# Kernel tuning notes

Measured on AMD Instinct MI355X. Metric: run time of the kernel, lower is better.

Reference implementation:

```python
import jax, jax.numpy as jnp
import numpy as np

N = 100_000        # total nodes (BN)
E = 1_600_000      # directed edges before bidirectionalization
B = 8              # graphs in batch
CFG = 1000         # configs per graph -> BC = 8000
N_OPS = 120
OP_EMB = 8
F_NODE = 140
H = 64
IN_DIMS = [F_NODE + OP_EMB, H, H]  # [148, 64, 64]


def setup_inputs() -> dict:
    key = jax.random.key(0)
    ks = iter(jax.random.split(key, 40))
    d = {}
    d["node_feat"] = jax.random.normal(next(ks), (N, F_NODE), dtype=jnp.float32)
    d["node_opcode"] = jax.random.randint(next(ks), (N,), 0, N_OPS)
    d["edge_index"] = jax.random.randint(next(ks), (E, 2), 0, N)
    d["config_feat"] = jax.random.normal(next(ks), (B * CFG, 24), dtype=jnp.float32)
    d["n_configs"] = jnp.full((B,), CFG, dtype=jnp.int32)
    d["batch"] = jnp.repeat(jnp.arange(B, dtype=jnp.int32), N // B)
    d["op_emb"] = jax.random.normal(next(ks), (N_OPS, OP_EMB), dtype=jnp.float32) * 0.1
    s = 0.05
    for l, din in enumerate(IN_DIMS):
        d[f"sage_wl{l}"] = jax.random.normal(next(ks), (din, din), dtype=jnp.float32) * s
        d[f"sage_bl{l}"] = jnp.zeros((din,), dtype=jnp.float32)
        d[f"sage_wr{l}"] = jax.random.normal(next(ks), (din, din), dtype=jnp.float32) * s
        d[f"lin_w{l}"] = jax.random.normal(next(ks), (2 * din, H), dtype=jnp.float32) * s
        d[f"lin_b{l}"] = jnp.zeros((H,), dtype=jnp.float32)
    d["post_w1"] = jax.random.normal(next(ks), (H + 24, H), dtype=jnp.float32) * s
    d["post_b1"] = jnp.zeros((H,), dtype=jnp.float32)
    d["post_w2"] = jax.random.normal(next(ks), (H, 1), dtype=jnp.float32) * s
    d["post_b2"] = jnp.zeros((1,), dtype=jnp.float32)
    return d


def _forward(node_feat, config_feat, op_emb, layer_params, post_w1, post_b1,
             post_w2, post_b2, node_opcode, edge_index, n_configs, batch):
    # Bidirectional edges: original + transposed (matches edge_index[..., [1,0]] cat)
    src = jnp.concatenate([edge_index[:, 0], edge_index[:, 1]])
    dst = jnp.concatenate([edge_index[:, 1], edge_index[:, 0]])
    deg = jax.ops.segment_sum(jnp.ones_like(dst, dtype=node_feat.dtype), dst,
                              num_segments=N)
    inv_deg = (1.0 / jnp.maximum(deg, 1.0))[:, None]  # zero-in-degree -> mean 0

    x = jnp.concatenate([node_feat, op_emb[node_opcode]], axis=-1)  # (N, 148)
    for (wl, bl, wr, lw, lb) in layer_params:
        # SAGEConv: mean-aggregate neighbor messages, + root transform
        agg = jax.ops.segment_sum(x[src], dst, num_segments=N) * inv_deg
        h = agg @ wl + bl + x @ wr
        # normalize=True -> L2 normalize (F.normalize, eps=1e-12)
        nrm = jnp.linalg.norm(h, axis=-1, keepdims=True)
        h = h / jnp.maximum(nrm, 1e-12)
        z = jnp.concatenate([h, x], axis=-1) @ lw + lb
        x = jax.nn.leaky_relu(z)  # negative_slope=0.01 as in torch default

    g = jax.ops.segment_sum(x, batch, num_segments=B)  # global_add_pool (B, 64)
    g = jnp.repeat(g, n_configs, axis=0, total_repeat_length=B * CFG)
    z = jnp.concatenate([g, config_feat], axis=-1)     # (BC, 88)
    z = jax.nn.leaky_relu(z @ post_w1 + post_b1)
    out = (z @ post_w2 + post_b2).squeeze(-1)          # (BC,)
    return out


def reference(node_feat, node_opcode, edge_index, config_feat, n_configs, batch,
              op_emb,
              sage_wl0, sage_bl0, sage_wr0, lin_w0, lin_b0,
              sage_wl1, sage_bl1, sage_wr1, lin_w1, lin_b1,
              sage_wl2, sage_bl2, sage_wr2, lin_w2, lin_b2,
              post_w1, post_b1, post_w2, post_b2):
    layer_params = [
        (sage_wl0, sage_bl0, sage_wr0, lin_w0, lin_b0),
        (sage_wl1, sage_bl1, sage_wr1, lin_w1, lin_b1),
        (sage_wl2, sage_bl2, sage_wr2, lin_w2, lin_b2),
    ]
    return _forward(node_feat, config_feat, op_emb, layer_params,
                    post_w1, post_b1, post_w2, post_b2,
                    node_opcode, edge_index, n_configs, batch)
```

## Files before the change

kernel.cpp:

```cpp
#include <hip/hip_runtime.h>
#include <cstdint>
#include <cstddef>


#define LRELU(v) ((v) > 0.f ? (v) : 0.01f * (v))

typedef __attribute__((ext_vector_type(8))) short bf16x8;
typedef __attribute__((ext_vector_type(4))) float f32x4;
typedef float floatx2 __attribute__((ext_vector_type(2)));

union U4B8 {
    uint4 u;
    bf16x8 b;
};

__device__ inline unsigned bf16_rn(float x) {
    unsigned u = __float_as_uint(x);
    return (u + 0x7fffu + ((u >> 16) & 1u)) >> 16;
}
__device__ inline unsigned pack2(float lo, float hi) {
    return bf16_rn(lo) | (bf16_rn(hi) << 16);
}
__device__ inline float2 up2(unsigned v) {
    return make_float2(__uint_as_float(v << 16), __uint_as_float(v & 0xffff0000u));
}

__device__ inline float e4m3_to_f32(unsigned b) {
    float v = __uint_as_float((b & 0x7fu) << 20) * 0x1p120f;
    return __uint_as_float(__float_as_uint(v) | ((b & 0x80u) << 24));
}

template <bool HI>
__device__ inline floatx2 fp8x2_dec(unsigned v) {
#if __has_builtin(__builtin_amdgcn_cvt_pk_f32_fp8)
    return __builtin_amdgcn_cvt_pk_f32_fp8((int)v, HI);
#else
    unsigned w = HI ? (v >> 16) : v;
    floatx2 r;
    r.x = e4m3_to_f32(w & 0xffu);
    r.y = e4m3_to_f32((w >> 8) & 0xffu);
    return r;
#endif
}

__device__ inline unsigned char f32_to_e4m3_sw(float f) {
    unsigned u = __float_as_uint(f);
    unsigned s = (u >> 24) & 0x80u;
    float a = fabsf(f);
    if (a > 448.f) a = 448.f;
    unsigned b = __float_as_uint(a);
    int exp = (int)(b >> 23) - 127;
    unsigned r;
    if (exp < -9) {
        r = 0;
    } else if (exp >= -6) {
        unsigned m = b & 0x7fffffu;
        unsigned keep = m >> 20;
        unsigned rb = (m >> 19) & 1u;
        unsigned sticky = (m & 0x7ffffu) ? 1u : 0u;
        unsigned inc = rb & (sticky | (keep & 1u));
        unsigned em = (((unsigned)(exp + 7)) << 3) | keep;
        em += inc;
        if (em > 0x7eu) em = 0x7eu;
        r = em;
    } else {
        float t = a * 512.f;
        int q = (int)(t + 0.5f);
        r = (q > 7) ? 0x08u : (unsigned)q;
    }
    return (unsigned char)(r | s);
}

__device__ inline unsigned fp8x4_enc(float f0, float f1, float f2, float f3) {
#if __has_builtin(__builtin_amdgcn_cvt_pk_fp8_f32)
    int pk = __builtin_amdgcn_cvt_pk_fp8_f32(f0, f1, 0, false);
    pk = __builtin_amdgcn_cvt_pk_fp8_f32(f2, f3, pk, true);
    return (unsigned)pk;
#else
    return (unsigned)f32_to_e4m3_sw(f0) | ((unsigned)f32_to_e4m3_sw(f1) << 8) |
           ((unsigned)f32_to_e4m3_sw(f2) << 16) | ((unsigned)f32_to_e4m3_sw(f3) << 24);
#endif
}

__global__ void k_concat(const float* __restrict__ nf, const int* __restrict__ opc,
                         const float* __restrict__ emb, unsigned* __restrict__ x0,
                         unsigned* __restrict__ x8, int n) {
    int idx = blockIdx.x * 256 + threadIdx.x;
    if (idx >= n * 40) return;
    int node = idx / 40;
    int u = idx - node * 40;
    float f[4];
#pragma unroll
    for (int j = 0; j < 4; j++) {
        int ft = 4 * u + j;
        float v = 0.f;
        if (ft < 140) v = nf[(size_t)node * 140 + ft];
        else if (ft < 148) v = emb[opc[node] * 8 + (ft - 140)];
        f[j] = v;
    }
    ((uint2*)x0)[idx] = make_uint2(pack2(f[0], f[1]), pack2(f[2], f[3]));
    x8[idx] = fp8x4_enc(f[0], f[1], f[2], f[3]);
}

__global__ void k_cvt8(const unsigned* __restrict__ xb, unsigned* __restrict__ x8,
                       int n) {
    int idx = blockIdx.x * 256 + threadIdx.x;
    if (idx >= n * 16) return;
    uint2 v = ((const uint2*)xb)[idx];
    float2 ab = up2(v.x);
    float2 cd = up2(v.y);
    x8[idx] = fp8x4_enc(ab.x, ab.y, cd.x, cd.y);
}

__global__ __launch_bounds__(256) void k_bh(const int* __restrict__ ei, int E,
                                            int NBUCK, int* __restrict__ bcnt) {
    __shared__ int h[1024];
    int t = threadIdx.x;
    for (int i = t; i < 1024; i += 256) h[i] = 0;
    __syncthreads();
    int e0 = blockIdx.x * 4096, e1 = min(E, e0 + 4096);
    for (int e = e0 + t; e < e1; e += 256) {
        int a = ei[2 * e], b = ei[2 * e + 1];
        atomicAdd(&h[b >> 7], 1);
        atomicAdd(&h[a >> 7], 1);
    }
    __syncthreads();
    for (int i = t; i < NBUCK; i += 256)
        if (h[i]) atomicAdd(&bcnt[i], h[i]);
}

__global__ void k_bscan(const int* __restrict__ bcnt, int NBUCK,
                        int* __restrict__ bo, int* __restrict__ bfill) {
    __shared__ int sm[1024];
    int t = threadIdx.x;
    int v = (t < NBUCK) ? bcnt[t] : 0;
    sm[t] = v;
    __syncthreads();
    for (int off = 1; off < 1024; off <<= 1) {
        int u = 0;
        if (t >= off) u = sm[t - off];
        __syncthreads();
        sm[t] += u;
        __syncthreads();
    }
    if (t < NBUCK) {
        int ex = sm[t] - v;
        bo[t] = ex;
        bfill[t] = ex;
    }
    if (t == NBUCK - 1) bo[NBUCK] = sm[t];
}

__global__ __launch_bounds__(256) void k_bscatter(const int* __restrict__ ei, int E,
                                                  int* __restrict__ bfill,
                                                  uint2* __restrict__ pairs) {
    __shared__ int hist[1024], lbo[1024], gb[1024], cur[1024];
    __shared__ int wsum[4];
    __shared__ int stageD[8192];
    __shared__ int stageS[8192];
    int t = threadIdx.x;
    for (int i = t; i < 1024; i += 256) hist[i] = 0;
    __syncthreads();
    int e0 = blockIdx.x * 4096, e1 = min(E, e0 + 4096);
    for (int e = e0 + t; e < e1; e += 256) {
        int a = ei[2 * e], b = ei[2 * e + 1];
        atomicAdd(&hist[b >> 7], 1);
        atomicAdd(&hist[a >> 7], 1);
    }
    __syncthreads();
    int b4 = t * 4;
    int c0 = hist[b4], c1 = hist[b4 + 1], c2 = hist[b4 + 2], c3 = hist[b4 + 3];
    int ms = c0 + c1 + c2 + c3;
    int lane = t & 63, wv = t >> 6;
    int v = ms;
#pragma unroll
    for (int off = 1; off < 64; off <<= 1) {
        int u = __shfl_up(v, off, 64);
        if (lane >= off) v += u;
    }
    if (lane == 63) wsum[wv] = v;
    __syncthreads();
    int wb = 0;
    for (int i = 0; i < wv; i++) wb += wsum[i];
    int ex = wb + v - ms;
    lbo[b4] = ex;
    lbo[b4 + 1] = ex + c0;
    lbo[b4 + 2] = ex + c0 + c1;
    lbo[b4 + 3] = ex + c0 + c1 + c2;
    if (c0) gb[b4 + 0] = atomicAdd(&bfill[b4 + 0], c0);
    if (c1) gb[b4 + 1] = atomicAdd(&bfill[b4 + 1], c1);
    if (c2) gb[b4 + 2] = atomicAdd(&bfill[b4 + 2], c2);
    if (c3) gb[b4 + 3] = atomicAdd(&bfill[b4 + 3], c3);
    cur[b4] = 0;
    cur[b4 + 1] = 0;
    cur[b4 + 2] = 0;
    cur[b4 + 3] = 0;
    __syncthreads();
    for (int e = e0 + t; e < e1; e += 256) {
        int a = ei[2 * e], b = ei[2 * e + 1];
        int bk = b >> 7;
        int r = atomicAdd(&cur[bk], 1);
        int p = lbo[bk] + r;
        stageD[p] = b;
        stageS[p] = a;
        bk = a >> 7;
        r = atomicAdd(&cur[bk], 1);
        p = lbo[bk] + r;
        stageD[p] = a;
        stageS[p] = b;
    }
    __syncthreads();
    int tot = 2 * (e1 - e0);
    for (int i = t; i < tot; i += 256) {
        int d = stageD[i];
        int bk = d >> 7;
        pairs[gb[bk] + (i - lbo[bk])] = make_uint2((unsigned)d, (unsigned)stageS[i]);
    }
}

__global__ __launch_bounds__(256) void k_bfinal(const uint2* __restrict__ pairs,
                                                const int* __restrict__ bo,
                                                int* __restrict__ rp,
                                                int* __restrict__ csr,
                                                float* __restrict__ invd,
                                                int N, int NBUCK) {
    __shared__ int hist[128], ls[128], cur[128];
    __shared__ unsigned outS[6144];
    int t = threadIdx.x;
    int bk = blockIdx.x;
    int n0 = bk << 7;
    int nn = min(128, N - n0);
    int base = bo[bk], cnt = bo[bk + 1] - base;
    if (t < 128) {
        hist[t] = 0;
        cur[t] = 0;
    }
    __syncthreads();
    for (int i = t; i < cnt; i += 256) atomicAdd(&hist[(int)pairs[base + i].x - n0], 1);
    __syncthreads();
    if (t == 0) {
        int run = 0;
        for (int i = 0; i < 128; i++) {
            ls[i] = run;
            run += hist[i];
        }
    }
    __syncthreads();
    if (t < nn) {
        int node = n0 + t;
        rp[node] = base + ls[t];
        invd[node] = 1.0f / fmaxf((float)hist[t], 1.0f);
    }
    if (bk == NBUCK - 1 && t == 0) rp[N] = base + cnt;
    bool inl = (cnt <= 6144);
    for (int i = t; i < cnt; i += 256) {
        uint2 pr = pairs[base + i];
        int loc = (int)pr.x - n0;
        int r = atomicAdd(&cur[loc], 1);
        int pos = ls[loc] + r;
        if (inl) outS[pos] = pr.y;
        else csr[base + pos] = (int)pr.y;
    }
    __syncthreads();
    if (inl)
        for (int i = t; i < cnt; i += 256) csr[base + i] = (int)outS[i];
}

__global__ __launch_bounds__(256) void k_agg160(
    const unsigned* __restrict__ x8, const int* __restrict__ rp,
    const int* __restrict__ csr, const float* __restrict__ invd,
    unsigned* __restrict__ agg, int n) {
    int wave = threadIdx.x >> 6;
    int l = threadIdx.x & 63;
    int node = blockIdx.x * 4 + wave;
    if (node >= n) return;
    int p = l & 31;
    int h = l >> 5;
    int eg = l >> 3;
    int eq = l & 7;
    float am[4] = {0.f, 0.f, 0.f, 0.f};
    float ae[4] = {0.f, 0.f, 0.f, 0.f};
    int s = rp[node], e2 = rp[node + 1];
    int j = s;
    for (; j + 8 <= e2; j += 8) {
#pragma unroll
        for (int i = 0; i < 4; i++) {
            int u = csr[j + 2 * i + h];
            unsigned v = x8[(size_t)u * 40 + p];
            floatx2 lo = fp8x2_dec<false>(v);
            floatx2 hi = fp8x2_dec<true>(v);
            am[0] += lo.x;
            am[1] += lo.y;
            am[2] += hi.x;
            am[3] += hi.y;
        }
        int ue = csr[j + eg];
        unsigned v = x8[(size_t)ue * 40 + 32 + eq];
        floatx2 lo = fp8x2_dec<false>(v);
        floatx2 hi = fp8x2_dec<true>(v);
        ae[0] += lo.x;
        ae[1] += lo.y;
        ae[2] += hi.x;
        ae[3] += hi.y;
    }
    for (; j < e2; j++) {
        int u = csr[j];
        if (l < 32) {
            unsigned v = x8[(size_t)u * 40 + p];
            floatx2 lo = fp8x2_dec<false>(v);
            floatx2 hi = fp8x2_dec<true>(v);
            am[0] += lo.x;
            am[1] += lo.y;
            am[2] += hi.x;
            am[3] += hi.y;
        } else if (l < 40) {
            unsigned v = x8[(size_t)u * 40 + 32 + eq];
            floatx2 lo = fp8x2_dec<false>(v);
            floatx2 hi = fp8x2_dec<true>(v);
            ae[0] += lo.x;
            ae[1] += lo.y;
            ae[2] += hi.x;
            ae[3] += hi.y;
        }
    }
#pragma unroll
    for (int r = 0; r < 4; r++) am[r] += __shfl_xor(am[r], 32, 64);
#pragma unroll
    for (int r = 0; r < 4; r++) {
        ae[r] += __shfl_xor(ae[r], 8, 64);
        ae[r] += __shfl_xor(ae[r], 16, 64);
        ae[r] += __shfl_xor(ae[r], 32, 64);
    }
    float iv = invd[node];
    unsigned* row = agg + (size_t)node * 80;
    if (l < 32)
        ((uint2*)row)[p] = make_uint2(pack2(am[0] * iv, am[1] * iv),
                                      pack2(am[2] * iv, am[3] * iv));
    if (l < 8)
        ((uint2*)(row + 64))[eq] = make_uint2(pack2(ae[0] * iv, ae[1] * iv),
                                              pack2(ae[2] * iv, ae[3] * iv));
}

__global__ __launch_bounds__(256) void k_agg64_8(
    const unsigned* __restrict__ x8, const int* __restrict__ rp,
    const int* __restrict__ csr, const float* __restrict__ invd,
    unsigned* __restrict__ agg, int n) {
    int wave = threadIdx.x >> 6;
    int l = threadIdx.x & 63;
    int node = blockIdx.x * 4 + wave;
    if (node >= n) return;
    int p = l & 15;
    int g = l >> 4;
    float a[4] = {0.f, 0.f, 0.f, 0.f};
    int s = rp[node], e2 = rp[node + 1];
    int j = s;
    for (; j + 8 <= e2; j += 8) {
        int u0 = csr[j + g];
        int u1 = csr[j + 4 + g];
        unsigned v0 = x8[(size_t)u0 * 16 + p];
        unsigned v1 = x8[(size_t)u1 * 16 + p];
        floatx2 lo0 = fp8x2_dec<false>(v0);
        floatx2 hi0 = fp8x2_dec<true>(v0);
        floatx2 lo1 = fp8x2_dec<false>(v1);
        floatx2 hi1 = fp8x2_dec<true>(v1);
        a[0] += lo0.x + lo1.x;
        a[1] += lo0.y + lo1.y;
        a[2] += hi0.x + hi1.x;
        a[3] += hi0.y + hi1.y;
    }
    for (; j < e2; j += 4) {
        if (j + g < e2) {
            int u = csr[j + g];
            unsigned v = x8[(size_t)u * 16 + p];
            floatx2 lo = fp8x2_dec<false>(v);
            floatx2 hi = fp8x2_dec<true>(v);
            a[0] += lo.x;
            a[1] += lo.y;
            a[2] += hi.x;
            a[3] += hi.y;
        }
    }
#pragma unroll
    for (int r = 0; r < 4; r++) {
        a[r] += __shfl_xor(a[r], 16, 64);
        a[r] += __shfl_xor(a[r], 32, 64);
    }
    if (l < 16) {
        float iv = invd[node];
        ((uint2*)(agg + (size_t)node * 32))[p] =
            make_uint2(pack2(a[0] * iv, a[1] * iv), pack2(a[2] * iv, a[3] * iv));
    }
}

template <int KS, int KSH, int CT, int C>
__global__ void k_prep(const float* __restrict__ W1, const float* __restrict__ W2,
                       int K1, int K2, uint4* __restrict__ Wp) {
    int idx = blockIdx.x * 256 + threadIdx.x;
    if (idx >= CT * KS * 64) return;
    int l = idx & 63;
    int ks = (idx >> 6) % KS;
    int ct = idx / (KS * 64);
    int col = ct * 16 + (l & 15);
    int kbase = ks * 32 + (l >> 4) * 8;
    unsigned short v[8];
#pragma unroll
    for (int j = 0; j < 8; j++) {
        int k = kbase + j;
        float f = 0.f;
        if (col < C) {
            if (k < KSH * 32) {
                if (k < K1) f = W1[(size_t)k * C + col];
            } else {
                int k2 = k - KSH * 32;
                if (k2 < K2) f = W2[(size_t)k2 * C + col];
            }
        }
        v[j] = (unsigned short)bf16_rn(f);
    }
    uint4 o;
    o.x = v[0] | ((unsigned)v[1] << 16);
    o.y = v[2] | ((unsigned)v[3] << 16);
    o.z = v[4] | ((unsigned)v[5] << 16);
    o.w = v[6] | ((unsigned)v[7] << 16);
    Wp[idx] = o;
}

template <int KS, int KSH, int CT, int C, int OST, int NORM, int ACT, int OUTF>
__global__ __launch_bounds__(256) void k_gemm(
    const uint4* __restrict__ A, const uint4* __restrict__ Bb,
    const uint4* __restrict__ Wp, const float* __restrict__ bias,
    void* __restrict__ outv, int n) {
    int l = threadIdx.x & 63;
    int wv = threadIdx.x >> 6;
    int rb = blockIdx.x * 64 + wv * 16;
    int rowA = rb + (l & 15);
    if (rowA >= n) rowA = n - 1;
    int koct = l >> 4;
    const int strideU = KSH * 4;
    size_t baseA = (size_t)rowA * strideU + koct;

    f32x4 acc[CT];
#pragma unroll
    for (int ct = 0; ct < CT; ct++) acc[ct] = (f32x4){0.f, 0.f, 0.f, 0.f};

#pragma unroll
    for (int ks = 0; ks < KS; ks++) {
        U4B8 a;
        a.u = (ks < KSH) ? A[baseA + ks * 4] : Bb[baseA + (ks - KSH) * 4];
#pragma unroll
        for (int ct = 0; ct < CT; ct++) {
            U4B8 b;
            b.u = Wp[(ct * KS + ks) * 64 + l];
            acc[ct] = __builtin_amdgcn_mfma_f32_16x16x32_bf16(a.b, b.b, acc[ct], 0, 0, 0);
        }
    }

    int cid = l & 15;
    int grp = l >> 4;
#pragma unroll
    for (int ct = 0; ct < CT; ct++) {
        int col = ct * 16 + cid;
        float bv = (col < C) ? bias[col] : 0.f;
#pragma unroll
        for (int r = 0; r < 4; r++) acc[ct][r] += bv;
    }

    if (NORM) {
        float ss[4];
#pragma unroll
        for (int r = 0; r < 4; r++) {
            ss[r] = 0.f;
#pragma unroll
            for (int ct = 0; ct < CT; ct++) ss[r] += acc[ct][r] * acc[ct][r];
        }
#pragma unroll
        for (int off = 1; off < 16; off <<= 1) {
#pragma unroll
            for (int r = 0; r < 4; r++) ss[r] += __shfl_xor(ss[r], off, 64);
        }
#pragma unroll
        for (int r = 0; r < 4; r++) {
            float sc = 1.0f / fmaxf(sqrtf(ss[r]), 1e-12f);
#pragma unroll
            for (int ct = 0; ct < CT; ct++) acc[ct][r] *= sc;
        }
    }

    if (ACT) {
#pragma unroll
        for (int ct = 0; ct < CT; ct++)
#pragma unroll
            for (int r = 0; r < 4; r++) acc[ct][r] = LRELU(acc[ct][r]);
    }

#pragma unroll
    for (int r = 0; r < 4; r++) {
        int row = rb + grp * 4 + r;
        if (row >= n) continue;
        if (OUTF) {
            float* o = (float*)outv;
#pragma unroll
            for (int ct = 0; ct < CT; ct++) {
                int col = ct * 16 + cid;
                if (col < OST) o[(size_t)row * OST + col] = acc[ct][r];
            }
        } else {
            unsigned short* o = (unsigned short*)outv;
#pragma unroll
            for (int ct = 0; ct < CT; ct++) {
                int col = ct * 16 + cid;
                if (col < OST) o[(size_t)row * OST + col] = (unsigned short)bf16_rn(acc[ct][r]);
            }
        }
    }
}

__global__ __launch_bounds__(256) void k_pool(const float* __restrict__ x,
                                              const int* __restrict__ batch,
                                              float* __restrict__ g, int n) {
    __shared__ float sm[8][64];
    __shared__ int sb[8];
    int lane = threadIdx.x & 63;
    int wv = threadIdx.x >> 6;
    int base = blockIdx.x * 256 + wv * 64;
    float a0 = 0.f, a1 = 0.f;
    int b0 = -1, b1 = -1;
    int end = (base + 64 < n) ? base + 64 : n;
    for (int row = base; row < end; row++) {
        int bg = batch[row];
        float v = x[(size_t)row * 64 + lane];
        if (b0 < 0) b0 = bg;
        if (bg == b0) a0 += v;
        else { if (b1 < 0) b1 = bg; a1 += v; }
    }
    sm[wv * 2 + 0][lane] = a0;
    sm[wv * 2 + 1][lane] = a1;
    if (lane == 0) {
        sb[wv * 2 + 0] = b0;
        sb[wv * 2 + 1] = b1;
    }
    __syncthreads();
    if (wv == 0) {
        float c0 = 0.f, c1 = 0.f;
        int d0 = -1, d1 = -1;
#pragma unroll
        for (int s = 0; s < 8; s++) {
            int bg = sb[s];
            if (bg < 0) continue;
            float v = sm[s][lane];
            if (d0 < 0) d0 = bg;
            if (bg == d0) c0 += v;
            else { if (d1 < 0) d1 = bg; c1 += v; }
        }
        if (d0 >= 0) atomicAdd(&g[d0 * 64 + lane], c0);
        if (d1 >= 0) atomicAdd(&g[d1 * 64 + lane], c1);
    }
}

__global__ void k_post1(const float* __restrict__ g, const float* __restrict__ cf,
                        const int* __restrict__ ncfg, const float* __restrict__ w1,
                        const float* __restrict__ b1, float* __restrict__ z,
                        int BC, int B) {
    int idx = blockIdx.x * 256 + threadIdx.x;
    if (idx >= BC * 64) return;
    int row = idx >> 6, c = idx & 63;
    int gsum = 0, gid = B - 1;
    for (int b2 = 0; b2 < B; b2++) {
        int ns = ncfg[b2];
        if (row < gsum + ns) { gid = b2; break; }
        gsum += ns;
    }
    float acc = b1[c];
#pragma unroll 4
    for (int k = 0; k < 64; k++) acc += g[gid * 64 + k] * w1[k * 64 + c];
#pragma unroll 4
    for (int k = 0; k < 24; k++) acc += cf[(size_t)row * 24 + k] * w1[(64 + k) * 64 + c];
    z[idx] = LRELU(acc);
}

__global__ void k_post2(const float* __restrict__ z, const float* __restrict__ w2,
                        const float* __restrict__ b2, float* __restrict__ out, int BC) {
    int row = blockIdx.x * 4 + (threadIdx.x >> 6);
    if (row >= BC) return;
    int c = threadIdx.x & 63;
    float v = z[(size_t)row * 64 + c] * w2[c];
#pragma unroll
    for (int off = 32; off > 0; off >>= 1) v += __shfl_xor(v, off, 64);
    if (c == 0) out[row] = v + b2[0];
}

extern "C" void kernel_launch(void* const* d_in, const int* in_sizes, int n_in,
                              void* d_out, int out_size, void* d_ws, size_t ws_size,
                              hipStream_t stream) {
    const float* node_feat = (const float*)d_in[0];
    const int*   opcode    = (const int*)d_in[1];
    const int*   ei        = (const int*)d_in[2];
    const float* cf        = (const float*)d_in[3];
    const int*   ncfg      = (const int*)d_in[4];
    const int*   batch     = (const int*)d_in[5];
    const float* emb       = (const float*)d_in[6];
    const float* wl0 = (const float*)d_in[7];
    const float* bl0 = (const float*)d_in[8];
    const float* wr0 = (const float*)d_in[9];
    const float* lw0 = (const float*)d_in[10];
    const float* lb0 = (const float*)d_in[11];
    const float* wl1 = (const float*)d_in[12];
    const float* bl1 = (const float*)d_in[13];
    const float* wr1 = (const float*)d_in[14];
    const float* lw1 = (const float*)d_in[15];
    const float* lb1 = (const float*)d_in[16];
    const float* wl2 = (const float*)d_in[17];
    const float* bl2 = (const float*)d_in[18];
    const float* wr2 = (const float*)d_in[19];
    const float* lw2 = (const float*)d_in[20];
    const float* lb2 = (const float*)d_in[21];
    const float* pw1 = (const float*)d_in[22];
    const float* pb1 = (const float*)d_in[23];
    const float* pw2 = (const float*)d_in[24];
    const float* pb2 = (const float*)d_in[25];

    const int N  = in_sizes[0] / 140;
    const int E  = in_sizes[2] / 2;
    const int B  = in_sizes[4];
    const int BC = in_sizes[3] / 24;
    const int NBUCK = (N + 127) >> 7;

    char* w = (char*)d_ws;
    auto alloc = [&](size_t bytes) {
        void* p = (void*)w;
        w += (bytes + 255) & ~(size_t)255;
        return p;
    };
    int*      bcnt     = (int*)alloc(1024 * 4);
    int*      bo       = (int*)alloc(1025 * 4);
    int*      bfill    = (int*)alloc(1024 * 4);
    uint2*    pairs    = (uint2*)alloc((size_t)2 * E * 8);
    int*      rp       = (int*)alloc((size_t)(N + 1) * 4);
    float*    invd     = (float*)alloc((size_t)N * 4);
    int*      csr      = (int*)alloc((size_t)2 * E * 4);
    unsigned* X0       = (unsigned*)alloc((size_t)N * 80 * 4);
    unsigned* AG0      = (unsigned*)alloc((size_t)N * 80 * 4);
    unsigned* H0       = (unsigned*)alloc((size_t)N * 80 * 4);
    unsigned* T0       = (unsigned*)alloc((size_t)N * 32 * 4);
    unsigned* T1       = (unsigned*)alloc((size_t)N * 32 * 4);
    unsigned* T2       = (unsigned*)alloc((size_t)N * 32 * 4);
    unsigned* G8       = (unsigned*)alloc((size_t)N * 16 * 4);
    float*    X3F      = (float*)alloc((size_t)N * 64 * 4);
    float*    gbuf     = (float*)alloc((size_t)B * 64 * 4);
    float*    zp       = (float*)alloc((size_t)BC * 64 * 4);
    uint4*    Wp0h     = (uint4*)alloc((size_t)10 * 10 * 64 * 16);
    uint4*    Wp0l     = (uint4*)alloc((size_t)4 * 10 * 64 * 16);
    uint4*    Wp1h     = (uint4*)alloc((size_t)4 * 4 * 64 * 16);
    uint4*    Wp1l     = (uint4*)alloc((size_t)4 * 4 * 64 * 16);
    uint4*    Wp2h     = (uint4*)alloc((size_t)4 * 4 * 64 * 16);
    uint4*    Wp2l     = (uint4*)alloc((size_t)4 * 4 * 64 * 16);
    unsigned* X08      = (unsigned*)pairs;
    (void)ws_size; (void)n_in; (void)out_size;

    (void)hipMemsetAsync(bcnt, 0, 1024 * 4, stream);
    (void)hipMemsetAsync(gbuf, 0, (size_t)B * 64 * 4, stream);

    k_prep<10, 5, 10, 148><<<(6400 + 255) / 256, 256, 0, stream>>>(wl0, wr0, 148, 148, Wp0h);
    k_prep<10, 5, 4, 64><<<(2560 + 255) / 256, 256, 0, stream>>>(lw0, lw0 + 148 * 64, 148, 148, Wp0l);
    k_prep<4, 2, 4, 64><<<4, 256, 0, stream>>>(wl1, wr1, 64, 64, Wp1h);
    k_prep<4, 2, 4, 64><<<4, 256, 0, stream>>>(lw1, lw1 + 64 * 64, 64, 64, Wp1l);
    k_prep<4, 2, 4, 64><<<4, 256, 0, stream>>>(wl2, wr2, 64, 64, Wp2h);
    k_prep<4, 2, 4, 64><<<4, 256, 0, stream>>>(lw2, lw2 + 64 * 64, 64, 64, Wp2l);

    const int EB = (E + 4095) / 4096;
    k_bh<<<EB, 256, 0, stream>>>(ei, E, NBUCK, bcnt);
    k_bscan<<<1, 1024, 0, stream>>>(bcnt, NBUCK, bo, bfill);
    k_bscatter<<<EB, 256, 0, stream>>>(ei, E, bfill, pairs);
    k_bfinal<<<NBUCK, 256, 0, stream>>>(pairs, bo, rp, csr, invd, N, NBUCK);

    k_concat<<<(N * 40 + 255) / 256, 256, 0, stream>>>(node_feat, opcode, emb, X0, X08, N);

    const int AGG_GRID  = (N + 3) / 4;
    const int GEMM_GRID = (N + 63) / 64;
    const int CVT_GRID  = (N * 16 + 255) / 256;

    k_agg160<<<AGG_GRID, 256, 0, stream>>>(X08, rp, csr, invd, AG0, N);
    k_gemm<10, 5, 10, 148, 160, 1, 0, 0><<<GEMM_GRID, 256, 0, stream>>>(
        (const uint4*)AG0, (const uint4*)X0, Wp0h, bl0, H0, N);
    k_gemm<10, 5, 4, 64, 64, 0, 1, 0><<<GEMM_GRID, 256, 0, stream>>>(
        (const uint4*)H0, (const uint4*)X0, Wp0l, lb0, T0, N);

    k_cvt8<<<CVT_GRID, 256, 0, stream>>>(T0, G8, N);
    k_agg64_8<<<AGG_GRID, 256, 0, stream>>>(G8, rp, csr, invd, T1, N);
    k_gemm<4, 2, 4, 64, 64, 1, 0, 0><<<GEMM_GRID, 256, 0, stream>>>(
        (const uint4*)T1, (const uint4*)T0, Wp1h, bl1, T2, N);
    k_gemm<4, 2, 4, 64, 64, 0, 1, 0><<<GEMM_GRID, 256, 0, stream>>>(
        (const uint4*)T2, (const uint4*)T0, Wp1l, lb1, T1, N);

    k_cvt8<<<CVT_GRID, 256, 0, stream>>>(T1, G8, N);
    k_agg64_8<<<AGG_GRID, 256, 0, stream>>>(G8, rp, csr, invd, T0, N);
    k_gemm<4, 2, 4, 64, 64, 1, 0, 0><<<GEMM_GRID, 256, 0, stream>>>(
        (const uint4*)T0, (const uint4*)T1, Wp2h, bl2, T2, N);
    k_gemm<4, 2, 4, 64, 64, 0, 1, 1><<<GEMM_GRID, 256, 0, stream>>>(
        (const uint4*)T2, (const uint4*)T1, Wp2l, lb2, X3F, N);

    k_pool<<<(N + 255) / 256, 256, 0, stream>>>(X3F, batch, gbuf, N);
    k_post1<<<(BC * 64 + 255) / 256, 256, 0, stream>>>(gbuf, cf, ncfg, pw1, pb1, zp, BC, B);
    k_post2<<<(BC + 3) / 4, 256, 0, stream>>>(zp, pw2, pb2, (float*)d_out, BC);
}
```

Measured before the change: 531.3 us.

## Split fp8 features into main/extra arrays, unroll agg64, and register-block GEMM rows

The layer-0 fp8 features are split into a 128-byte main array and a separate 32-byte extra array, so gathers of the main part touch aligned 128-byte rows instead of 160-byte rows. The 64-wide aggregation gets a 16-edge unrolled loop that issues four independent gathers before decoding, for more memory-level parallelism. The GEMM kernel now computes two 16-row fragments per wave and reuses each weight fragment load across both, halving the grid. This adds register pressure, which may lower occupancy.

```diff
diff --git a/kernel.cpp b/kernel.cpp
--- a/kernel.cpp
+++ b/kernel.cpp
@@ -84,7 +84,8 @@
 
 __global__ void k_concat(const float* __restrict__ nf, const int* __restrict__ opc,
                          const float* __restrict__ emb, unsigned* __restrict__ x0,
-                         unsigned* __restrict__ x8, int n) {
+                         unsigned* __restrict__ m8, unsigned* __restrict__ e8,
+                         int n) {
     int idx = blockIdx.x * 256 + threadIdx.x;
     if (idx >= n * 40) return;
     int node = idx / 40;
@@ -99,7 +100,9 @@
         f[j] = v;
     }
     ((uint2*)x0)[idx] = make_uint2(pack2(f[0], f[1]), pack2(f[2], f[3]));
-    x8[idx] = fp8x4_enc(f[0], f[1], f[2], f[3]);
+    unsigned enc = fp8x4_enc(f[0], f[1], f[2], f[3]);
+    if (u < 32) m8[(size_t)node * 32 + u] = enc;
+    else        e8[(size_t)node * 8 + (u - 32)] = enc;
 }
 
 __global__ void k_cvt8(const unsigned* __restrict__ xb, unsigned* __restrict__ x8,
@@ -267,9 +270,9 @@
 }
 
 __global__ __launch_bounds__(256) void k_agg160(
-    const unsigned* __restrict__ x8, const int* __restrict__ rp,
-    const int* __restrict__ csr, const float* __restrict__ invd,
-    unsigned* __restrict__ agg, int n) {
+    const unsigned* __restrict__ m8, const unsigned* __restrict__ e8,
+    const int* __restrict__ rp, const int* __restrict__ csr,
+    const float* __restrict__ invd, unsigned* __restrict__ agg, int n) {
     int wave = threadIdx.x >> 6;
     int l = threadIdx.x & 63;
     int node = blockIdx.x * 4 + wave;
@@ -286,7 +289,7 @@
 #pragma unroll
         for (int i = 0; i < 4; i++) {
             int u = csr[j + 2 * i + h];
-            unsigned v = x8[(size_t)u * 40 + p];
+            unsigned v = m8[(size_t)u * 32 + p];
             floatx2 lo = fp8x2_dec<false>(v);
             floatx2 hi = fp8x2_dec<true>(v);
             am[0] += lo.x;
@@ -295,7 +298,7 @@
             am[3] += hi.y;
         }
         int ue = csr[j + eg];
-        unsigned v = x8[(size_t)ue * 40 + 32 + eq];
+        unsigned v = e8[(size_t)ue * 8 + eq];
         floatx2 lo = fp8x2_dec<false>(v);
         floatx2 hi = fp8x2_dec<true>(v);
         ae[0] += lo.x;
@@ -306,7 +309,7 @@
     for (; j < e2; j++) {
         int u = csr[j];
         if (l < 32) {
-            unsigned v = x8[(size_t)u * 40 + p];
+            unsigned v = m8[(size_t)u * 32 + p];
             floatx2 lo = fp8x2_dec<false>(v);
             floatx2 hi = fp8x2_dec<true>(v);
             am[0] += lo.x;
@@ -314,7 +317,7 @@
             am[2] += hi.x;
             am[3] += hi.y;
         } else if (l < 40) {
-            unsigned v = x8[(size_t)u * 40 + 32 + eq];
+            unsigned v = e8[(size_t)u * 8 + eq];
             floatx2 lo = fp8x2_dec<false>(v);
             floatx2 hi = fp8x2_dec<true>(v);
             ae[0] += lo.x;
@@ -354,6 +357,23 @@
     float a[4] = {0.f, 0.f, 0.f, 0.f};
     int s = rp[node], e2 = rp[node + 1];
     int j = s;
+    for (; j + 16 <= e2; j += 16) {
+        unsigned v[4];
+#pragma unroll
+        for (int i = 0; i < 4; i++) {
+            int u = csr[j + 4 * i + g];
+            v[i] = x8[(size_t)u * 16 + p];
+        }
+#pragma unroll
+        for (int i = 0; i < 4; i++) {
+            floatx2 lo = fp8x2_dec<false>(v[i]);
+            floatx2 hi = fp8x2_dec<true>(v[i]);
+            a[0] += lo.x;
+            a[1] += lo.y;
+            a[2] += hi.x;
+            a[3] += hi.y;
+        }
+    }
     for (; j + 8 <= e2; j += 8) {
         int u0 = csr[j + g];
         int u1 = csr[j + 4 + g];
@@ -425,91 +445,109 @@
     Wp[idx] = o;
 }
 
-template <int KS, int KSH, int CT, int C, int OST, int NORM, int ACT, int OUTF>
+template <int KS, int KSH, int CT, int C, int OST, int NORM, int ACT, int OUTF,
+          int RF>
 __global__ __launch_bounds__(256) void k_gemm(
     const uint4* __restrict__ A, const uint4* __restrict__ Bb,
     const uint4* __restrict__ Wp, const float* __restrict__ bias,
     void* __restrict__ outv, int n) {
     int l = threadIdx.x & 63;
     int wv = threadIdx.x >> 6;
-    int rb = blockIdx.x * 64 + wv * 16;
-    int rowA = rb + (l & 15);
-    if (rowA >= n) rowA = n - 1;
+    constexpr int WROWS = 16 * RF;
+    int rb = blockIdx.x * (4 * WROWS) + wv * WROWS;
     int koct = l >> 4;
     const int strideU = KSH * 4;
-    size_t baseA = (size_t)rowA * strideU + koct;
-
-    f32x4 acc[CT];
-#pragma unroll
-    for (int ct = 0; ct < CT; ct++) acc[ct] = (f32x4){0.f, 0.f, 0.f, 0.f};
+    size_t baseA[RF];
+#pragma unroll
+    for (int rf = 0; rf < RF; rf++) {
+        int rowA = rb + rf * 16 + (l & 15);
+        if (rowA >= n) rowA = n - 1;
+        baseA[rf] = (size_t)rowA * strideU + koct;
+    }
+
+    f32x4 acc[RF][CT];
+#pragma unroll
+    for (int rf = 0; rf < RF; rf++)
+#pragma unroll
+        for (int ct = 0; ct < CT; ct++) acc[rf][ct] = (f32x4){0.f, 0.f, 0.f, 0.f};
 
 #pragma unroll
     for (int ks = 0; ks < KS; ks++) {
-        U4B8 a;
-        a.u = (ks < KSH) ? A[baseA + ks * 4] : Bb[baseA + (ks - KSH) * 4];
+        U4B8 a[RF];
+#pragma unroll
+        for (int rf = 0; rf < RF; rf++)
+            a[rf].u = (ks < KSH) ? A[baseA[rf] + ks * 4]
+                                 : Bb[baseA[rf] + (ks - KSH) * 4];
 #pragma unroll
         for (int ct = 0; ct < CT; ct++) {
             U4B8 b;
             b.u = Wp[(ct * KS + ks) * 64 + l];
-            acc[ct] = __builtin_amdgcn_mfma_f32_16x16x32_bf16(a.b, b.b, acc[ct], 0, 0, 0);
+#pragma unroll
+            for (int rf = 0; rf < RF; rf++)
+                acc[rf][ct] = __builtin_amdgcn_mfma_f32_16x16x32_bf16(
+                    a[rf].b, b.b, acc[rf][ct], 0, 0, 0);
         }
     }
 
     int cid = l & 15;
     int grp = l >> 4;
 #pragma unroll
-    for (int ct = 0; ct < CT; ct++) {
-        int col = ct * 16 + cid;
-        float bv = (col < C) ? bias[col] : 0.f;
-#pragma unroll
-        for (int r = 0; r < 4; r++) acc[ct][r] += bv;
-    }
-
-    if (NORM) {
-        float ss[4];
+    for (int rf = 0; rf < RF; rf++) {
+#pragma unroll
+        for (int ct = 0; ct < CT; ct++) {
+            int col = ct * 16 + cid;
+            float bv = (col < C) ? bias[col] : 0.f;
+#pragma unroll
+            for (int r = 0; r < 4; r++) acc[rf][ct][r] += bv;
+        }
+
+        if (NORM) {
+            float ss[4];
+#pragma unroll
+            for (int r = 0; r < 4; r++) {
+                ss[r] = 0.f;
+#pragma unroll
+                for (int ct = 0; ct < CT; ct++) ss[r] += acc[rf][ct][r] * acc[rf][ct][r];
+            }
+#pragma unroll
+            for (int off = 1; off < 16; off <<= 1) {
+#pragma unroll
+                for (int r = 0; r < 4; r++) ss[r] += __shfl_xor(ss[r], off, 64);
+            }
+#pragma unroll
+            for (int r = 0; r < 4; r++) {
+                float sc = 1.0f / fmaxf(sqrtf(ss[r]), 1e-12f);
+#pragma unroll
+                for (int ct = 0; ct < CT; ct++) acc[rf][ct][r] *= sc;
+            }
+        }
+
+        if (ACT) {
+#pragma unroll
+            for (int ct = 0; ct < CT; ct++)
+#pragma unroll
+                for (int r = 0; r < 4; r++) acc[rf][ct][r] = LRELU(acc[rf][ct][r]);
+        }
+
 #pragma unroll
         for (int r = 0; r < 4; r++) {
-            ss[r] = 0.f;
-#pragma unroll
-            for (int ct = 0; ct < CT; ct++) ss[r] += acc[ct][r] * acc[ct][r];
-        }
-#pragma unroll
-        for (int off = 1; off < 16; off <<= 1) {
-#pragma unroll
-            for (int r = 0; r < 4; r++) ss[r] += __shfl_xor(ss[r], off, 64);
-        }
-#pragma unroll
-        for (int r = 0; r < 4; r++) {
-            float sc = 1.0f / fmaxf(sqrtf(ss[r]), 1e-12f);
-#pragma unroll
-            for (int ct = 0; ct < CT; ct++) acc[ct][r] *= sc;
-        }
-    }
-
-    if (ACT) {
-#pragma unroll
-        for (int ct = 0; ct < CT; ct++)
-#pragma unroll
-            for (int r = 0; r < 4; r++) acc[ct][r] = LRELU(acc[ct][r]);
-    }
-
-#pragma unroll
-    for (int r = 0; r < 4; r++) {
-        int row = rb + grp * 4 + r;
-        if (row >= n) continue;
-        if (OUTF) {
-            float* o = (float*)outv;
-#pragma unroll
-            for (int ct = 0; ct < CT; ct++) {
-                int col = ct * 16 + cid;
-                if (col < OST) o[(size_t)row * OST + col] = acc[ct][r];
-            }
-        } else {
-            unsigned short* o = (unsigned short*)outv;
-#pragma unroll
-            for (int ct = 0; ct < CT; ct++) {
-                int col = ct * 16 + cid;
-                if (col < OST) o[(size_t)row * OST + col] = (unsigned short)bf16_rn(acc[ct][r]);
+            int row = rb + rf * 16 + grp * 4 + r;
+            if (row >= n) continue;
+            if (OUTF) {
+                float* o = (float*)outv;
+#pragma unroll
+                for (int ct = 0; ct < CT; ct++) {
+                    int col = ct * 16 + cid;
+                    if (col < OST) o[(size_t)row * OST + col] = acc[rf][ct][r];
+                }
+            } else {
+                unsigned short* o = (unsigned short*)outv;
+#pragma unroll
+                for (int ct = 0; ct < CT; ct++) {
+                    int col = ct * 16 + cid;
+                    if (col < OST)
+                        o[(size_t)row * OST + col] = (unsigned short)bf16_rn(acc[rf][ct][r]);
+                }
             }
         }
     }
@@ -654,7 +692,8 @@
     uint4*    Wp1l     = (uint4*)alloc((size_t)4 * 4 * 64 * 16);
     uint4*    Wp2h     = (uint4*)alloc((size_t)4 * 4 * 64 * 16);
     uint4*    Wp2l     = (uint4*)alloc((size_t)4 * 4 * 64 * 16);
-    unsigned* X08      = (unsigned*)pairs;
+    unsigned* M8       = (unsigned*)pairs;
+    unsigned* E8       = M8 + (size_t)N * 32;
     (void)ws_size; (void)n_in; (void)out_size;
 
     (void)hipMemsetAsync(bcnt, 0, 1024 * 4, stream);
@@ -673,30 +712,30 @@
     k_bscatter<<<EB, 256, 0, stream>>>(ei, E, bfill, pairs);
     k_bfinal<<<NBUCK, 256, 0, stream>>>(pairs, bo, rp, csr, invd, N, NBUCK);
 
-    k_concat<<<(N * 40 + 255) / 256, 256, 0, stream>>>(node_feat, opcode, emb, X0, X08, N);
-
-    const int AGG_GRID  = (N + 3) / 4;
-    const int GEMM_GRID = (N + 63) / 64;
-    const int CVT_GRID  = (N * 16 + 255) / 256;
-
-    k_agg160<<<AGG_GRID, 256, 0, stream>>>(X08, rp, csr, invd, AG0, N);
-    k_gemm<10, 5, 10, 148, 160, 1, 0, 0><<<GEMM_GRID, 256, 0, stream>>>(
+    k_concat<<<(N * 40 + 255) / 256, 256, 0, stream>>>(node_feat, opcode, emb, X0, M8, E8, N);
+
+    const int AGG_GRID   = (N + 3) / 4;
+    const int GEMM_GRID2 = (N + 127) / 128;
+    const int CVT_GRID   = (N * 16 + 255) / 256;
+
+    k_agg160<<<AGG_GRID, 256, 0, stream>>>(M8, E8, rp, csr, invd, AG0, N);
+    k_gemm<10, 5, 10, 148, 160, 1, 0, 0, 2><<<GEMM_GRID2, 256, 0, stream>>>(
         (const uint4*)AG0, (const uint4*)X0, Wp0h, bl0, H0, N);
-    k_gemm<10, 5, 4, 64, 64, 0, 1, 0><<<GEMM_GRID, 256, 0, stream>>>(
+    k_gemm<10, 5, 4, 64, 64, 0, 1, 0, 2><<<GEMM_GRID2, 256, 0, stream>>>(
         (const uint4*)H0, (const uint4*)X0, Wp0l, lb0, T0, N);
 
     k_cvt8<<<CVT_GRID, 256, 0, stream>>>(T0, G8, N);
     k_agg64_8<<<AGG_GRID, 256, 0, stream>>>(G8, rp, csr, invd, T1, N);
-    k_gemm<4, 2, 4, 64, 64, 1, 0, 0><<<GEMM_GRID, 256, 0, stream>>>(
+    k_gemm<4, 2, 4, 64, 64, 1, 0, 0, 2><<<GEMM_GRID2, 256, 0, stream>>>(
         (const uint4*)T1, (const uint4*)T0, Wp1h, bl1, T2, N);
-    k_gemm<4, 2, 4, 64, 64, 0, 1, 0><<<GEMM_GRID, 256, 0, stream>>>(
+    k_gemm<4, 2, 4, 64, 64, 0, 1, 0, 2><<<GEMM_GRID2, 256, 0, stream>>>(
         (const uint4*)T2, (const uint4*)T0, Wp1l, lb1, T1, N);
 
     k_cvt8<<<CVT_GRID, 256, 0, stream>>>(T1, G8, N);
     k_agg64_8<<<AGG_GRID, 256, 0, stream>>>(G8, rp, csr, invd, T0, N);
-    k_gemm<4, 2, 4, 64, 64, 1, 0, 0><<<GEMM_GRID, 256, 0, stream>>>(
+    k_gemm<4, 2, 4, 64, 64, 1, 0, 0, 2><<<GEMM_GRID2, 256, 0, stream>>>(
         (const uint4*)T0, (const uint4*)T1, Wp2h, bl2, T2, N);
-    k_gemm<4, 2, 4, 64, 64, 0, 1, 1><<<GEMM_GRID, 256, 0, stream>>>(
+    k_gemm<4, 2, 4, 64, 64, 0, 1, 1, 2><<<GEMM_GRID2, 256, 0, stream>>>(
         (const uint4*)T2, (const uint4*)T1, Wp2l, lb2, X3F, N);
 
     k_pool<<<(N + 255) / 256, 256, 0, stream>>>(X3F, batch, gbuf, N);
```

Result: no change. 531.1 us (-0.0%).
